# Performance work log

Measured on AMD Instinct MI355X. Metric: run time of the kernel, lower is better.

Reference implementation:

```python
import jax, jax.numpy as jnp
import numpy as np

N = 100000   # nodes
E = 1600000  # edges (avg degree 16)
D = 64       # input feature dim


def _lin(k, i, o):
    return (jax.random.normal(k, (i, o), jnp.float32) / np.float32(np.sqrt(i)))


def setup_inputs() -> dict:
    key = jax.random.key(0)
    ks = jax.random.split(key, 12)
    return {
        "x": jax.random.normal(ks[0], (N, D), jnp.float32),
        "edge_index": jax.random.randint(ks[1], (2, E), 0, N, dtype=jnp.int64),
        # layer 1: SAGEConv(64, 64, 'pool')
        "W1_pool": _lin(ks[2], 64, 64), "b1_pool": jnp.zeros((64,), jnp.float32),
        "W1_self": _lin(ks[3], 64, 64), "W1_neigh": _lin(ks[4], 64, 64),
        "b1": jnp.zeros((64,), jnp.float32),
        # layer 2: SAGEConv(64, 32, 'pool')
        "W2_pool": _lin(ks[5], 64, 64), "b2_pool": jnp.zeros((64,), jnp.float32),
        "W2_self": _lin(ks[6], 64, 32), "W2_neigh": _lin(ks[7], 64, 32),
        "b2": jnp.zeros((32,), jnp.float32),
        # layer 3: SAGEConv(32, 32, 'mean')
        "W3_self": _lin(ks[8], 32, 32), "W3_neigh": _lin(ks[9], 32, 32),
        "b3": jnp.zeros((32,), jnp.float32),
    }


def _sage_pool(x, src, dst, Wp, bp, Ws, Wn, b):
    # max-pool aggregator: transform all nodes once (cheaper than per-edge),
    # gather per-edge, segment-max into destination nodes.
    m = jax.nn.relu(x @ Wp + bp)[src]                      # [E, in]
    agg = jax.ops.segment_max(m, dst, num_segments=N)     # [N, in]
    agg = jnp.where(jnp.isfinite(agg), agg, jnp.float32(0.0))  # isolated nodes -> 0
    return x @ Ws + agg @ Wn + b


def _sage_mean(x, src, dst, Ws, Wn, b):
    s = jax.ops.segment_sum(x[src], dst, num_segments=N)   # [N, in]
    cnt = jax.ops.segment_sum(jnp.ones((src.shape[0],), jnp.float32), dst,
                              num_segments=N)
    agg = s / jnp.maximum(cnt, jnp.float32(1.0))[:, None]
    return x @ Ws + agg @ Wn + b


def reference(x, edge_index,
              W1_pool, b1_pool, W1_self, W1_neigh, b1,
              W2_pool, b2_pool, W2_self, W2_neigh, b2,
              W3_self, W3_neigh, b3):
    src, dst = edge_index[0], edge_index[1]
    h = jax.nn.relu(_sage_pool(x, src, dst, W1_pool, b1_pool, W1_self, W1_neigh, b1))
    h = _sage_pool(h, src, dst, W2_pool, b2_pool, W2_self, W2_neigh, b2)
    h = _sage_mean(h, src, dst, W3_self, W3_neigh, b3)
    return h
```

## Files before the change

kernel.cpp:

```cpp
#include <hip/hip_runtime.h>
#include <hip/hip_bf16.h>


typedef unsigned int uint;
typedef short short8 __attribute__((ext_vector_type(8)));
typedef float f32x4 __attribute__((ext_vector_type(4)));
typedef float f32x2 __attribute__((ext_vector_type(2)));
typedef unsigned short u16x8 __attribute__((ext_vector_type(8)));

__device__ __forceinline__ float bf2f(unsigned short h){
  return __uint_as_float(((uint)h) << 16);
}
__device__ __forceinline__ unsigned short f2bf(float f){
  uint u = __float_as_uint(f);
  u += 0x7fffu + ((u >> 16) & 1u);
  return (unsigned short)(u >> 16);
}
__device__ __forceinline__ float lo16(uint u){ return __uint_as_float(u << 16); }
__device__ __forceinline__ float hi16(uint u){ return __uint_as_float(u & 0xffff0000u); }

__device__ __forceinline__ uint4 pkmax4(uint4 a, uint4 b){
  u16x8 x = __builtin_bit_cast(u16x8, a);
  u16x8 y = __builtin_bit_cast(u16x8, b);
  return __builtin_bit_cast(uint4, __builtin_elementwise_max(x, y));
}
__device__ __forceinline__ uint4 shflx4(uint4 a, int off){
  uint4 r;
  r.x = (uint)__shfl_xor((int)a.x, off, 64);
  r.y = (uint)__shfl_xor((int)a.y, off, 64);
  r.z = (uint)__shfl_xor((int)a.z, off, 64);
  r.w = (uint)__shfl_xor((int)a.w, off, 64);
  return r;
}
__device__ __forceinline__ f32x2 b2lo(uint u){
  f32x2 r; r.x = lo16(u); r.y = hi16(u); return r;
}

struct WConv {
  const void* src[13];
  int n[13], isbias[13], Cs[13], K[13], off[13];
};

__global__ void conv_w(WConv wc, unsigned short* wtbase, float* bbase,
                       const unsigned short* x, const int* ei,
                       int* flags, int* ccur, int NB){
  __shared__ int sflags[2];
  int t = threadIdx.x;
  if (t < 64){
    int sane = 0;
    #pragma unroll
    for (int k = 0; k < 4; ++k){
      int e = (x[(t * 4 + k) * 2] >> 7) & 0xff;
      sane += (e >= 118 && e <= 134);
    }
    #pragma unroll
    for (int off = 32; off; off >>= 1) sane += __shfl_down(sane, off, 64);
    unsigned long long b = __ballot(ei[1 + 2 * t] != 0);
    if (t == 0){ sflags[0] = (sane >= 128); sflags[1] = (b == 0ull); }
  }
  __syncthreads();
  int isbf = sflags[0];
  if (blockIdx.x == 0){
    if (t == 0){ flags[0] = sflags[0]; flags[1] = sflags[1]; }
    for (int i = t; i < NB; i += 256) ccur[i] = 0;
  }
  int bt = blockIdx.x, n = wc.n[bt];
  if (wc.isbias[bt]){
    float* d = bbase + wc.off[bt];
    for (int i = t; i < n; i += 256)
      d[i] = isbf ? bf2f(((const unsigned short*)wc.src[bt])[i])
                  : ((const float*)wc.src[bt])[i];
  } else {
    unsigned short* d = wtbase + wc.off[bt];
    int Cs = wc.Cs[bt], K = wc.K[bt], Cm = (1 << Cs) - 1;
    for (int i = t; i < n; i += 256){
      int k = i >> Cs, c = i & Cm;
      unsigned short v = isbf ? ((const unsigned short*)wc.src[bt])[i]
                              : f2bf(((const float*)wc.src[bt])[i]);
      d[c * K + k] = v;
    }
  }
}

__device__ __forceinline__ void load_edge(const void* ei, int E, int is64, int e,
                                          int& s, int& d){
  if (is64){
    const long long* p = (const long long*)ei;
    s = (int)p[e]; d = (int)p[E + e];
  } else {
    const int* p = (const int*)ei;
    s = p[e]; d = p[E + e];
  }
}

__device__ __forceinline__ short8 ld_fragA_bf16(const unsigned short* A, int row,
                                                int K, int koff){
  return *(const short8*)(A + (size_t)row * K + koff);
}
__device__ __forceinline__ short8 ld_fragA_f32(const float* A, int row,
                                               int K, int koff){
  const float* q = A + (size_t)row * K + koff;
  float4 f0 = *(const float4*)q;
  float4 f1 = *(const float4*)(q + 4);
  short8 r;
  r[0] = (short)f2bf(f0.x); r[1] = (short)f2bf(f0.y);
  r[2] = (short)f2bf(f0.z); r[3] = (short)f2bf(f0.w);
  r[4] = (short)f2bf(f1.x); r[5] = (short)f2bf(f1.y);
  r[6] = (short)f2bf(f1.z); r[7] = (short)f2bf(f1.w);
  return r;
}
__device__ __forceinline__ unsigned short f2bf_relu(float f){
  return (unsigned short)(f2bf(fmaxf(f, 0.f)) & 0x7fff);
}

#define CSR_CE 2048

__device__ __forceinline__ void phase1_body(
    const void* __restrict__ ei, const int* __restrict__ flags,
    int* __restrict__ ccur, uint* __restrict__ pairs,
    int E, int N, int NB, int S, int CAP, int blk,
    uint* hist, uint* gbase)
{
  int t = threadIdx.x;
  uint dmask = (1u << S) - 1u;
  int is64 = flags[1];
  int e0 = blk * CSR_CE;
  for (int i = t; i < 1024; i += 256) hist[i] = 0;
  __syncthreads();
  uint pr[8]; short bb[8];
  #pragma unroll
  for (int k = 0; k < 8; ++k){
    int e = e0 + k * 256 + t;
    int s = 0, d = 0; bool ok = (e < E);
    if (ok){
      load_edge(ei, E, is64, e, s, d);
      ok = (unsigned)s < (unsigned)N && (unsigned)d < (unsigned)N;
    }
    bb[k] = ok ? (short)(d >> S) : (short)(-1);
    pr[k] = ((uint)s << S) | ((uint)d & dmask);
    if (ok) atomicAdd(&hist[d >> S], 1u);
  }
  __syncthreads();
  for (int b = t; b < NB; b += 256){
    uint c = hist[b];
    if (c) gbase[b] = (uint)atomicAdd(&ccur[b], (int)c);
    hist[b] = 0;
  }
  __syncthreads();
  #pragma unroll
  for (int k = 0; k < 8; ++k){
    int b = (int)bb[k];
    if (b >= 0){
      uint local = atomicAdd(&hist[b], 1u);
      uint pos = gbase[b] + local;
      if (pos >= (uint)CAP) pos = (uint)CAP - 1;
      pairs[(size_t)b * CAP + pos] = pr[k];
    }
  }
}

template<int AMODE>
__device__ __forceinline__ void mm1_body(
    const void* __restrict__ Av, const unsigned short* __restrict__ WaT,
    const float* __restrict__ bias, const int* __restrict__ flags,
    unsigned short* __restrict__ out, int N, int blk)
{
  int wid = threadIdx.x >> 6, lane = threadIdx.x & 63;
  int n0 = blk * 32;
  int m = lane & 15, quad = lane >> 4, koq = quad * 8;
  int colbase = wid * 16;
  int rowc0 = min(n0 + m, N - 1);
  int rowc1 = min(n0 + 16 + m, N - 1);
  bool af32 = (AMODE == 2) && (flags[0] == 0);
  f32x4 a0 = {0.f,0.f,0.f,0.f}, a1 = {0.f,0.f,0.f,0.f};
  #pragma unroll
  for (int k0 = 0; k0 < 64; k0 += 32){
    short8 af0 = af32 ? ld_fragA_f32((const float*)Av, rowc0, 64, k0 + koq)
                      : ld_fragA_bf16((const unsigned short*)Av, rowc0, 64, k0 + koq);
    short8 af1 = af32 ? ld_fragA_f32((const float*)Av, rowc1, 64, k0 + koq)
                      : ld_fragA_bf16((const unsigned short*)Av, rowc1, 64, k0 + koq);
    short8 wf = *(const short8*)(WaT + (size_t)(colbase + m) * 64 + k0 + koq);
    a0 = __builtin_amdgcn_mfma_f32_16x16x32_bf16(af0, wf, a0, 0, 0, 0);
    a1 = __builtin_amdgcn_mfma_f32_16x16x32_bf16(af1, wf, a1, 0, 0, 0);
  }
  float bv = bias[colbase + m];
  #pragma unroll
  for (int r = 0; r < 4; ++r){
    int rl = quad * 4 + r;
    if (n0 + rl < N)
      out[(size_t)(n0 + rl) * 64 + colbase + m] = f2bf_relu(a0[r] + bv);
    if (n0 + 16 + rl < N)
      out[(size_t)(n0 + 16 + rl) * 64 + colbase + m] = f2bf_relu(a1[r] + bv);
  }
}

template<int AMODE>
__global__ __launch_bounds__(256) void phase1_mm1(
    const void* __restrict__ ei, const int* __restrict__ flags,
    int* __restrict__ ccur, uint* __restrict__ pairs,
    int E, int N, int NB, int S, int CAP, int nP,
    const void* __restrict__ x, const unsigned short* __restrict__ W1pT,
    const float* __restrict__ b1p, unsigned short* __restrict__ mbuf)
{
  __shared__ uint hist[1024];
  __shared__ uint gbase[1024];
  if ((int)blockIdx.x < nP)
    phase1_body(ei, flags, ccur, pairs, E, N, NB, S, CAP, blockIdx.x, hist, gbase);
  else
    mm1_body<AMODE>(x, W1pT, b1p, flags, mbuf, N, blockIdx.x - nP);
}

__global__ void csr_scan0(const int* __restrict__ ccur, int* __restrict__ cbase,
                          int* __restrict__ rowptrN, int NB, int CAP)
{
  __shared__ int sm[256];
  int t = threadIdx.x;
  int g = (NB + 255) / 256;
  int vb = t * g, v[4], s = 0;
  for (int k = 0; k < g; ++k){
    int i = vb + k; int x = (i < NB) ? min(ccur[i], CAP) : 0; v[k] = x; s += x;
  }
  sm[t] = s; __syncthreads();
  for (int off = 1; off < 256; off <<= 1){
    int x = (t >= off) ? sm[t - off] : 0;
    __syncthreads(); sm[t] += x; __syncthreads();
  }
  int run = sm[t] - s;
  for (int k = 0; k < g; ++k){
    int i = vb + k;
    if (i < NB){ cbase[i] = run; run += v[k]; }
  }
  if (t == 255){ cbase[NB] = run; *rowptrN = run; }
}

#define P2_CAP 6144
__global__ __launch_bounds__(256) void csr_phase2(
    const int* __restrict__ cbase, const int* __restrict__ ccur,
    const uint* __restrict__ pairs,
    int* __restrict__ bucket, int* __restrict__ row_ptr, int N, int S, int CAP)
{
  __shared__ int lbuf[P2_CAP];
  __shared__ int cur[1024];
  __shared__ int sm[256];
  int b = blockIdx.x, t = threadIdx.x;
  uint dmask = (1u << S) - 1u;
  int n0 = b << S;
  int n1 = n0 + (1 << S); if (n1 > N) n1 = N;
  int nn = n1 - n0;
  int base = cbase[b];
  int cnt = min(ccur[b], CAP);
  const uint* bp = pairs + (size_t)b * CAP;

  for (int i = t; i < nn; i += 256) cur[i] = 0;
  __syncthreads();
  for (int j = t; j < cnt; j += 256)
    atomicAdd(&cur[(int)(bp[j] & dmask)], 1);
  __syncthreads();
  int g = (nn + 255) / 256, vb = t * g, v[4], s = 0;
  for (int k = 0; k < g; ++k){
    int i = vb + k; int x = (i < nn) ? cur[i] : 0; v[k] = x; s += x;
  }
  sm[t] = s; __syncthreads();
  for (int off = 1; off < 256; off <<= 1){
    int x = (t >= off) ? sm[t - off] : 0;
    __syncthreads(); sm[t] += x; __syncthreads();
  }
  int run = sm[t] - s;
  for (int k = 0; k < g; ++k){
    int i = vb + k;
    if (i < nn){ row_ptr[n0 + i] = base + run; cur[i] = run; run += v[k]; }
  }
  __syncthreads();
  if (cnt <= 0) return;
  if (cnt <= P2_CAP){
    for (int j = t; j < cnt; j += 256){
      uint pr = bp[j];
      int pos = atomicAdd(&cur[(int)(pr & dmask)], 1);
      lbuf[pos] = (int)(pr >> S);
    }
    __syncthreads();
    for (int i = t; i < cnt; i += 256) bucket[base + i] = lbuf[i];
  } else {
    for (int j = t; j < cnt; j += 256){
      uint pr = bp[j];
      int pos = atomicAdd(&cur[(int)(pr & dmask)], 1);
      bucket[base + pos] = (int)(pr >> S);
    }
  }
}

__global__ __launch_bounds__(256) void gather_max64(
    const int* __restrict__ row_ptr, const int* __restrict__ bucket,
    const unsigned short* __restrict__ m, unsigned short* __restrict__ agg, int N)
{
  int wave = (int)((blockIdx.x * 256u + threadIdx.x) >> 6);
  int lane = threadIdx.x & 63;
  int nodeA = wave * 2, nodeB = nodeA + 1;
  if (nodeA >= N) return;
  bool hasB = nodeB < N;
  int rsA = row_ptr[nodeA], reA = row_ptr[nodeA + 1];
  int cntA = reA - rsA;
  int rsB = reA, cntB = hasB ? (row_ptr[nodeB + 1] - reA) : 0;
  int fg8 = (lane & 7) * 8, rowsel = lane >> 3;
  uint4 accA = {0u,0u,0u,0u}, accB = {0u,0u,0u,0u};
  int cmax = max(cntA, cntB);
  for (int c0 = 0; c0 < cmax; c0 += 64){
    int chA = min(cntA - c0, 64);
    int chB = min(cntB - c0, 64);
    int bvA = (lane < chA) ? bucket[rsA + c0 + lane] : 0;
    int bvB = (lane < chB) ? bucket[rsB + c0 + lane] : 0;
    int it = (max(chA, chB) + 7) >> 3;
    for (int k = 0; k < it; ++k){
      int j = k * 8 + rowsel;
      int sA = __shfl(bvA, j, 64);
      int sB = __shfl(bvB, j, 64);
      uint4 vA = *(const uint4*)(m + (size_t)sA * 64 + fg8);
      uint4 vB = *(const uint4*)(m + (size_t)sB * 64 + fg8);
      if (j < chA) accA = pkmax4(accA, vA);
      if (j < chB) accB = pkmax4(accB, vB);
    }
  }
  #pragma unroll
  for (int off = 8; off <= 32; off <<= 1){
    accA = pkmax4(accA, shflx4(accA, off));
    accB = pkmax4(accB, shflx4(accB, off));
  }
  if (lane < 8){
    *(uint4*)(agg + (size_t)nodeA * 64 + fg8) = accA;
  } else if (lane < 16 && hasB){
    *(uint4*)(agg + (size_t)nodeB * 64 + (lane & 7) * 8) = accB;
  }
}

template<int AMODE>
__global__ __launch_bounds__(256) void mfma_mm_fused(
    const void* __restrict__ Av, const unsigned short* __restrict__ Bv,
    const unsigned short* __restrict__ WaT, const unsigned short* __restrict__ WbT,
    const float* __restrict__ bias1,
    const unsigned short* __restrict__ WcT, const float* __restrict__ bias2,
    const int* __restrict__ flags,
    unsigned short* __restrict__ out1, unsigned short* __restrict__ out2, int N)
{
  constexpr int K = 64, C = 64, LDH = 72;
  __shared__ unsigned short hl[32 * LDH];
  int wid = threadIdx.x >> 6, lane = threadIdx.x & 63;
  int n0 = blockIdx.x * 32;
  int m = lane & 15, quad = lane >> 4, koq = quad * 8;
  int colbase = wid * 16;
  int rowc0 = min(n0 + m, N - 1);
  int rowc1 = min(n0 + 16 + m, N - 1);
  bool af32 = (AMODE == 2) && (flags[0] == 0);

  f32x4 a0 = {0.f,0.f,0.f,0.f}, a1 = {0.f,0.f,0.f,0.f};
  #pragma unroll
  for (int k0 = 0; k0 < K; k0 += 32){
    short8 af0 = af32 ? ld_fragA_f32((const float*)Av, rowc0, K, k0 + koq)
                      : ld_fragA_bf16((const unsigned short*)Av, rowc0, K, k0 + koq);
    short8 af1 = af32 ? ld_fragA_f32((const float*)Av, rowc1, K, k0 + koq)
                      : ld_fragA_bf16((const unsigned short*)Av, rowc1, K, k0 + koq);
    short8 wf = *(const short8*)(WaT + (size_t)(colbase + m) * K + k0 + koq);
    a0 = __builtin_amdgcn_mfma_f32_16x16x32_bf16(af0, wf, a0, 0, 0, 0);
    a1 = __builtin_amdgcn_mfma_f32_16x16x32_bf16(af1, wf, a1, 0, 0, 0);
    short8 bf0 = ld_fragA_bf16(Bv, rowc0, K, k0 + koq);
    short8 bf1 = ld_fragA_bf16(Bv, rowc1, K, k0 + koq);
    short8 wg = *(const short8*)(WbT + (size_t)(colbase + m) * K + k0 + koq);
    a0 = __builtin_amdgcn_mfma_f32_16x16x32_bf16(bf0, wg, a0, 0, 0, 0);
    a1 = __builtin_amdgcn_mfma_f32_16x16x32_bf16(bf1, wg, a1, 0, 0, 0);
  }
  float bv = bias1[colbase + m];
  #pragma unroll
  for (int r = 0; r < 4; ++r){
    int rl = quad * 4 + r;
    unsigned short h0 = f2bf_relu(a0[r] + bv);
    unsigned short h1v = f2bf_relu(a1[r] + bv);
    hl[rl * LDH + colbase + m] = h0;
    hl[(16 + rl) * LDH + colbase + m] = h1v;
    if (n0 + rl < N) out1[(size_t)(n0 + rl) * C + colbase + m] = h0;
    if (n0 + 16 + rl < N) out1[(size_t)(n0 + 16 + rl) * C + colbase + m] = h1v;
  }
  __syncthreads();
  f32x4 c0 = {0.f,0.f,0.f,0.f}, c1 = {0.f,0.f,0.f,0.f};
  #pragma unroll
  for (int k0 = 0; k0 < K; k0 += 32){
    short8 q0 = *(const short8*)(hl + m * LDH + k0 + koq);
    short8 q1 = *(const short8*)(hl + (16 + m) * LDH + k0 + koq);
    short8 wf = *(const short8*)(WcT + (size_t)(colbase + m) * K + k0 + koq);
    c0 = __builtin_amdgcn_mfma_f32_16x16x32_bf16(q0, wf, c0, 0, 0, 0);
    c1 = __builtin_amdgcn_mfma_f32_16x16x32_bf16(q1, wf, c1, 0, 0, 0);
  }
  float b2v = bias2[colbase + m];
  #pragma unroll
  for (int r = 0; r < 4; ++r){
    int rl = quad * 4 + r;
    if (n0 + rl < N)
      out2[(size_t)(n0 + rl) * C + colbase + m] = f2bf_relu(c0[r] + b2v);
    if (n0 + 16 + rl < N)
      out2[(size_t)(n0 + 16 + rl) * C + colbase + m] = f2bf_relu(c1[r] + b2v);
  }
}

__global__ __launch_bounds__(256) void mfma_mm2(
    const unsigned short* __restrict__ h1, const unsigned short* __restrict__ aggb,
    const unsigned short* __restrict__ WsT, const unsigned short* __restrict__ WnT,
    const float* __restrict__ bias, unsigned short* __restrict__ h2, int N)
{
  int wid = threadIdx.x >> 6, lane = threadIdx.x & 63;
  int n0 = blockIdx.x * 64 + (wid >> 1) * 32;
  int colbase = (wid & 1) * 16;
  int m = lane & 15, quad = lane >> 4, koq = quad * 8;
  int rowc0 = min(n0 + m, N - 1), rowc1 = min(n0 + 16 + m, N - 1);
  f32x4 a0 = {0.f,0.f,0.f,0.f}, a1 = {0.f,0.f,0.f,0.f};
  #pragma unroll
  for (int k0 = 0; k0 < 64; k0 += 32){
    short8 af0 = *(const short8*)(h1 + (size_t)rowc0 * 64 + k0 + koq);
    short8 af1 = *(const short8*)(h1 + (size_t)rowc1 * 64 + k0 + koq);
    short8 wf = *(const short8*)(WsT + (size_t)(colbase + m) * 64 + k0 + koq);
    a0 = __builtin_amdgcn_mfma_f32_16x16x32_bf16(af0, wf, a0, 0, 0, 0);
    a1 = __builtin_amdgcn_mfma_f32_16x16x32_bf16(af1, wf, a1, 0, 0, 0);
    short8 bf0 = *(const short8*)(aggb + (size_t)rowc0 * 64 + k0 + koq);
    short8 bf1 = *(const short8*)(aggb + (size_t)rowc1 * 64 + k0 + koq);
    short8 wg = *(const short8*)(WnT + (size_t)(colbase + m) * 64 + k0 + koq);
    a0 = __builtin_amdgcn_mfma_f32_16x16x32_bf16(bf0, wg, a0, 0, 0, 0);
    a1 = __builtin_amdgcn_mfma_f32_16x16x32_bf16(bf1, wg, a1, 0, 0, 0);
  }
  float bv = bias[colbase + m];
  #pragma unroll
  for (int r = 0; r < 4; ++r){
    int rl = quad * 4 + r;
    if (n0 + rl < N)
      h2[(size_t)(n0 + rl) * 32 + colbase + m] = f2bf(a0[r] + bv);
    if (n0 + 16 + rl < N)
      h2[(size_t)(n0 + 16 + rl) * 32 + colbase + m] = f2bf(a1[r] + bv);
  }
}

__global__ __launch_bounds__(256) void gsum3(
    const int* __restrict__ row_ptr, const int* __restrict__ bucket,
    const unsigned short* __restrict__ h2,
    const unsigned short* __restrict__ W3sT, const unsigned short* __restrict__ W3nT,
    const float* __restrict__ b3, float* __restrict__ out, int N)
{
  constexpr int LDA = 40;
  __shared__ unsigned short la[16 * LDA];
  int t = threadIdx.x;
  int w = t >> 6, lane = t & 63;
  int n0 = blockIdx.x * 16;
  int g = lane >> 4, q = lane & 15;
  int nd = n0 + w * 4 + g;
  int ndc = nd < N ? nd : N - 1;
  int rs = row_ptr[ndc];
  int cnt = (nd < N) ? (row_ptr[ndc + 1] - rs) : 0;
  int fg8 = (q & 3) * 8, rowsel = q >> 2;
  f32x2 a0 = {0.f,0.f}, a1 = {0.f,0.f}, a2 = {0.f,0.f}, a3 = {0.f,0.f};
  for (int c0 = 0; c0 < cnt; c0 += 16){
    int chunk = min(cnt - c0, 16);
    int bval = (q < chunk) ? bucket[rs + c0 + q] : 0;
    int it = (chunk + 3) >> 2;
    for (int k = 0; k < it; ++k){
      int j = k * 4 + rowsel;
      int s = __shfl(bval, (g << 4) + j, 64);
      uint4 v = *(const uint4*)(h2 + (size_t)s * 32 + fg8);
      if (j < chunk){
        a0 += b2lo(v.x); a1 += b2lo(v.y); a2 += b2lo(v.z); a3 += b2lo(v.w);
      }
    }
  }
  #pragma unroll
  for (int off = 4; off <= 8; off <<= 1){
    a0.x += __shfl_xor(a0.x, off, 64); a0.y += __shfl_xor(a0.y, off, 64);
    a1.x += __shfl_xor(a1.x, off, 64); a1.y += __shfl_xor(a1.y, off, 64);
    a2.x += __shfl_xor(a2.x, off, 64); a2.y += __shfl_xor(a2.y, off, 64);
    a3.x += __shfl_xor(a3.x, off, 64); a3.y += __shfl_xor(a3.y, off, 64);
  }
  if (rowsel == 0){
    float sc = 1.f / fmaxf((float)cnt, 1.f);
    int r = w * 4 + g;
    uint4 pk;
    pk.x = (uint)f2bf(a0.x * sc) | ((uint)f2bf(a0.y * sc) << 16);
    pk.y = (uint)f2bf(a1.x * sc) | ((uint)f2bf(a1.y * sc) << 16);
    pk.z = (uint)f2bf(a2.x * sc) | ((uint)f2bf(a2.y * sc) << 16);
    pk.w = (uint)f2bf(a3.x * sc) | ((uint)f2bf(a3.y * sc) << 16);
    *(uint4*)(la + r * LDA + q * 8) = pk;
  }
  __syncthreads();
  if (w < 2){
    int m = lane & 15, quad = lane >> 4, koq = quad * 8;
    int colbase = w * 16;
    int row = n0 + m;
    int rowc = row < N ? row : N - 1;
    f32x4 acc = {0.f, 0.f, 0.f, 0.f};
    short8 aself = *(const short8*)(h2 + (size_t)rowc * 32 + koq);
    short8 wfs = *(const short8*)(W3sT + (size_t)(colbase + m) * 32 + koq);
    acc = __builtin_amdgcn_mfma_f32_16x16x32_bf16(aself, wfs, acc, 0, 0, 0);
    short8 aagg = *(const short8*)(la + m * LDA + koq);
    short8 wfn = *(const short8*)(W3nT + (size_t)(colbase + m) * 32 + koq);
    acc = __builtin_amdgcn_mfma_f32_16x16x32_bf16(aagg, wfn, acc, 0, 0, 0);
    float bv = b3[colbase + m];
    #pragma unroll
    for (int r = 0; r < 4; ++r){
      int orow = n0 + quad * 4 + r;
      if (orow < N) out[(size_t)orow * 32 + colbase + m] = acc[r] + bv;
    }
  }
}

static inline char* align256(char* p){
  return (char*)(((uintptr_t)p + 255) & ~(uintptr_t)255);
}

extern "C" void kernel_launch(void* const* d_in, const int* in_sizes, int n_in,
                              void* d_out, int out_size, void* d_ws, size_t ws_size,
                              hipStream_t stream)
{
  const void* x = d_in[0];
  const void* ei = d_in[1];
  int N = in_sizes[0] / 64;
  int E = in_sizes[1] / 2;

  char* ws = (char*)d_ws;
  unsigned short* wtbase = (unsigned short*)ws;
  float* bbase = (float*)(ws + 65536);
  int* flags = (int*)(ws + 131072 - 256);

  int S = 7, NB = (N + 127) >> 7;
  while (NB > 1024){ S++; NB = (N + (1 << S) - 1) >> S; }
  int CAP = ((2 * E / NB) + 255) & ~255;
  if (CAP < 1024) CAP = 1024;

  char* p = ws + 131072;
  int* row_ptr = (int*)p; p = align256(p + (size_t)(N + 1) * 4);
  int* cbase   = (int*)p; p = align256(p + 4352);
  int* ccur    = (int*)p; p = align256(p + 4352);
  int* bucket  = (int*)p; p = align256(p + (size_t)E * 4);
  uint* pairs  = (uint*)p; p = align256(p + (size_t)NB * CAP * 4);
  char* P = p;  p = align256(p + (size_t)N * 64 * 2);
  char* Q = p;  p = align256(p + (size_t)N * 64 * 2);
  char* R = p;  p = align256(p + (size_t)N * 64 * 2);
  unsigned short* mbuf = (unsigned short*)P;
  unsigned short* h2   = (unsigned short*)P;
  unsigned short* aggb = (unsigned short*)Q;
  unsigned short* h1   = (unsigned short*)R;

  WConv wc;
  {
    const int widx[13] = {2, 3, 4, 5, 6, 7, 8, 9, 10, 11, 12, 13, 14};
    const int isb[13]  = {0, 1, 0, 0, 1, 0, 1, 0, 0, 1, 0, 0, 1};
    const int Cs[13]   = {6, 0, 6, 6, 0, 6, 0, 5, 5, 0, 5, 5, 0};
    const int Kk[13]   = {64, 0, 64, 64, 0, 64, 0, 64, 64, 0, 32, 32, 0};
    const int off[13]  = {0, 0, 4096, 8192, 64, 12288, 128, 16384, 18432, 192,
                          20480, 21504, 224};
    for (int i = 0; i < 13; ++i){
      wc.src[i] = d_in[widx[i]]; wc.n[i] = in_sizes[widx[i]];
      wc.isbias[i] = isb[i]; wc.Cs[i] = Cs[i]; wc.K[i] = Kk[i]; wc.off[i] = off[i];
    }
  }
  hipLaunchKernelGGL(conv_w, dim3(13), dim3(256), 0, stream, wc, wtbase, bbase,
                     (const unsigned short*)x, (const int*)ei, flags, ccur, NB);
  unsigned short* W1pT = wtbase + 0;     unsigned short* W1sT = wtbase + 4096;
  unsigned short* W1nT = wtbase + 8192;  unsigned short* W2pT = wtbase + 12288;
  unsigned short* W2sT = wtbase + 16384; unsigned short* W2nT = wtbase + 18432;
  unsigned short* W3sT = wtbase + 20480; unsigned short* W3nT = wtbase + 21504;
  float* b1p = bbase + 0;  float* b1 = bbase + 64; float* b2p = bbase + 128;
  float* b2 = bbase + 192; float* b3 = bbase + 224;

  int nP = (E + CSR_CE - 1) / CSR_CE;
  int RT32 = (N + 31) / 32;
  int RT16 = (N + 15) / 16;
  int gg = (N + 7) / 8;

  phase1_mm1<2><<<nP + RT32, 256, 0, stream>>>(
      ei, flags, ccur, pairs, E, N, NB, S, CAP, nP, x, W1pT, b1p, mbuf);
  csr_scan0<<<1, 256, 0, stream>>>(ccur, cbase, row_ptr + N, NB, CAP);
  csr_phase2<<<NB, 256, 0, stream>>>(cbase, ccur, pairs, bucket, row_ptr, N, S, CAP);

  gather_max64<<<gg,256,0,stream>>>(row_ptr, bucket, mbuf, aggb, N);
  mfma_mm_fused<2><<<RT32,256,0,stream>>>(
      x, aggb, W1sT, W1nT, b1, W2pT, b2p, flags, h1, mbuf, N);

  gather_max64<<<gg,256,0,stream>>>(row_ptr, bucket, mbuf, aggb, N);
  mfma_mm2<<<(N + 63) / 64,256,0,stream>>>(h1, aggb, W2sT, W2nT, b2, h2, N);

  gsum3<<<RT16,256,0,stream>>>(row_ptr, bucket, h2, W3sT, W3nT, b3,
                               (float*)d_out, N);
}
```

Measured before the change: 292.3 us.

## Fuse max-gather into matmul kernels and enlarge CSR edge chunks

The two standalone gather_max64 kernels are folded into the following MFMA matmul kernels. Each block now gathers its own rows' neighbour max into shared memory and reads the aggregated operand from LDS, so the agg buffer no longer makes a global round trip and two launches are dropped. The layer-2 message buffer moves to its own allocation because m1 is read while m2 is written. CSR phase 1 now handles 8192 edges per block and re-reads edges in its second pass instead of holding them in registers, which means fewer blocks and fewer global atomics but twice the edge reads and less parallelism.

```diff
diff --git a/kernel.cpp b/kernel.cpp
--- a/kernel.cpp
+++ b/kernel.cpp
@@ -113,7 +113,7 @@
   return (unsigned short)(f2bf(fmaxf(f, 0.f)) & 0x7fff);
 }
 
-#define CSR_CE 2048
+#define CSR_CE 8192
 
 __device__ __forceinline__ void phase1_body(
     const void* __restrict__ ei, const int* __restrict__ flags,
@@ -127,18 +127,13 @@
   int e0 = blk * CSR_CE;
   for (int i = t; i < 1024; i += 256) hist[i] = 0;
   __syncthreads();
-  uint pr[8]; short bb[8];
-  #pragma unroll
-  for (int k = 0; k < 8; ++k){
-    int e = e0 + k * 256 + t;
-    int s = 0, d = 0; bool ok = (e < E);
-    if (ok){
-      load_edge(ei, E, is64, e, s, d);
-      ok = (unsigned)s < (unsigned)N && (unsigned)d < (unsigned)N;
-    }
-    bb[k] = ok ? (short)(d >> S) : (short)(-1);
-    pr[k] = ((uint)s << S) | ((uint)d & dmask);
-    if (ok) atomicAdd(&hist[d >> S], 1u);
+  #pragma unroll 4
+  for (int it = 0; it < CSR_CE / 256; ++it){
+    int e = e0 + it * 256 + t;
+    if (e >= E) break;
+    int s, d; load_edge(ei, E, is64, e, s, d);
+    if ((unsigned)s >= (unsigned)N || (unsigned)d >= (unsigned)N) continue;
+    atomicAdd(&hist[d >> S], 1u);
   }
   __syncthreads();
   for (int b = t; b < NB; b += 256){
@@ -147,15 +142,17 @@
     hist[b] = 0;
   }
   __syncthreads();
-  #pragma unroll
-  for (int k = 0; k < 8; ++k){
-    int b = (int)bb[k];
-    if (b >= 0){
-      uint local = atomicAdd(&hist[b], 1u);
-      uint pos = gbase[b] + local;
-      if (pos >= (uint)CAP) pos = (uint)CAP - 1;
-      pairs[(size_t)b * CAP + pos] = pr[k];
-    }
+  #pragma unroll 4
+  for (int it = 0; it < CSR_CE / 256; ++it){
+    int e = e0 + it * 256 + t;
+    if (e >= E) break;
+    int s, d; load_edge(ei, E, is64, e, s, d);
+    if ((unsigned)s >= (unsigned)N || (unsigned)d >= (unsigned)N) continue;
+    int b = d >> S;
+    uint local = atomicAdd(&hist[b], 1u);
+    uint pos = gbase[b] + local;
+    if (pos >= (uint)CAP) pos = (uint)CAP - 1;
+    pairs[(size_t)b * CAP + pos] = ((uint)s << S) | ((uint)d & dmask);
   }
 }
 
@@ -289,18 +286,17 @@
   }
 }
 
-__global__ __launch_bounds__(256) void gather_max64(
+__device__ __forceinline__ void gmax_pair(
     const int* __restrict__ row_ptr, const int* __restrict__ bucket,
-    const unsigned short* __restrict__ m, unsigned short* __restrict__ agg, int N)
-{
-  int wave = (int)((blockIdx.x * 256u + threadIdx.x) >> 6);
-  int lane = threadIdx.x & 63;
-  int nodeA = wave * 2, nodeB = nodeA + 1;
-  if (nodeA >= N) return;
-  bool hasB = nodeB < N;
-  int rsA = row_ptr[nodeA], reA = row_ptr[nodeA + 1];
-  int cntA = reA - rsA;
-  int rsB = reA, cntB = hasB ? (row_ptr[nodeB + 1] - reA) : 0;
+    const unsigned short* __restrict__ m,
+    unsigned short* la_row, int LDH, int nodeA, int N, int lane)
+{
+  int nodeB = nodeA + 1;
+  int nAc = min(nodeA, N - 1);
+  int rsA = row_ptr[nAc], reA = row_ptr[nAc + 1];
+  int cntA = (nodeA < N) ? (reA - rsA) : 0;
+  int rsB = reA;
+  int cntB = (nodeB < N) ? (row_ptr[nodeB + 1] - reA) : 0;
   int fg8 = (lane & 7) * 8, rowsel = lane >> 3;
   uint4 accA = {0u,0u,0u,0u}, accB = {0u,0u,0u,0u};
   int cmax = max(cntA, cntB);
@@ -326,15 +322,16 @@
     accB = pkmax4(accB, shflx4(accB, off));
   }
   if (lane < 8){
-    *(uint4*)(agg + (size_t)nodeA * 64 + fg8) = accA;
-  } else if (lane < 16 && hasB){
-    *(uint4*)(agg + (size_t)nodeB * 64 + (lane & 7) * 8) = accB;
+    *(uint4*)(la_row + fg8) = accA;
+  } else if (lane < 16){
+    *(uint4*)(la_row + LDH + (lane & 7) * 8) = accB;
   }
 }
 
 template<int AMODE>
-__global__ __launch_bounds__(256) void mfma_mm_fused(
-    const void* __restrict__ Av, const unsigned short* __restrict__ Bv,
+__global__ __launch_bounds__(256) void gmax_mm_fused(
+    const void* __restrict__ Av, const unsigned short* __restrict__ msrc,
+    const int* __restrict__ row_ptr, const int* __restrict__ bucket,
     const unsigned short* __restrict__ WaT, const unsigned short* __restrict__ WbT,
     const float* __restrict__ bias1,
     const unsigned short* __restrict__ WcT, const float* __restrict__ bias2,
@@ -342,9 +339,16 @@
     unsigned short* __restrict__ out1, unsigned short* __restrict__ out2, int N)
 {
   constexpr int K = 64, C = 64, LDH = 72;
+  __shared__ unsigned short la[32 * LDH];
   __shared__ unsigned short hl[32 * LDH];
   int wid = threadIdx.x >> 6, lane = threadIdx.x & 63;
   int n0 = blockIdx.x * 32;
+  #pragma unroll
+  for (int p = 0; p < 4; ++p){
+    int lr = wid * 8 + p * 2;
+    gmax_pair(row_ptr, bucket, msrc, la + (size_t)lr * LDH, LDH, n0 + lr, N, lane);
+  }
+  __syncthreads();
   int m = lane & 15, quad = lane >> 4, koq = quad * 8;
   int colbase = wid * 16;
   int rowc0 = min(n0 + m, N - 1);
@@ -361,8 +365,8 @@
     short8 wf = *(const short8*)(WaT + (size_t)(colbase + m) * K + k0 + koq);
     a0 = __builtin_amdgcn_mfma_f32_16x16x32_bf16(af0, wf, a0, 0, 0, 0);
     a1 = __builtin_amdgcn_mfma_f32_16x16x32_bf16(af1, wf, a1, 0, 0, 0);
-    short8 bf0 = ld_fragA_bf16(Bv, rowc0, K, k0 + koq);
-    short8 bf1 = ld_fragA_bf16(Bv, rowc1, K, k0 + koq);
+    short8 bf0 = *(const short8*)(la + m * LDH + k0 + koq);
+    short8 bf1 = *(const short8*)(la + (16 + m) * LDH + k0 + koq);
     short8 wg = *(const short8*)(WbT + (size_t)(colbase + m) * K + k0 + koq);
     a0 = __builtin_amdgcn_mfma_f32_16x16x32_bf16(bf0, wg, a0, 0, 0, 0);
     a1 = __builtin_amdgcn_mfma_f32_16x16x32_bf16(bf1, wg, a1, 0, 0, 0);
@@ -399,16 +403,26 @@
   }
 }
 
-__global__ __launch_bounds__(256) void mfma_mm2(
-    const unsigned short* __restrict__ h1, const unsigned short* __restrict__ aggb,
+__global__ __launch_bounds__(256) void gmax_mm2(
+    const unsigned short* __restrict__ h1, const unsigned short* __restrict__ msrc,
+    const int* __restrict__ row_ptr, const int* __restrict__ bucket,
     const unsigned short* __restrict__ WsT, const unsigned short* __restrict__ WnT,
     const float* __restrict__ bias, unsigned short* __restrict__ h2, int N)
 {
+  constexpr int LDH = 72;
+  __shared__ unsigned short la[64 * LDH];
   int wid = threadIdx.x >> 6, lane = threadIdx.x & 63;
-  int n0 = blockIdx.x * 64 + (wid >> 1) * 32;
+  int n0 = blockIdx.x * 64;
+  #pragma unroll
+  for (int p = 0; p < 8; ++p){
+    int lr = wid * 16 + p * 2;
+    gmax_pair(row_ptr, bucket, msrc, la + (size_t)lr * LDH, LDH, n0 + lr, N, lane);
+  }
+  __syncthreads();
+  int m = lane & 15, quad = lane >> 4, koq = quad * 8;
   int colbase = (wid & 1) * 16;
-  int m = lane & 15, quad = lane >> 4, koq = quad * 8;
-  int rowc0 = min(n0 + m, N - 1), rowc1 = min(n0 + 16 + m, N - 1);
+  int rb = (wid >> 1) * 32;
+  int rowc0 = min(n0 + rb + m, N - 1), rowc1 = min(n0 + rb + 16 + m, N - 1);
   f32x4 a0 = {0.f,0.f,0.f,0.f}, a1 = {0.f,0.f,0.f,0.f};
   #pragma unroll
   for (int k0 = 0; k0 < 64; k0 += 32){
@@ -417,8 +431,8 @@
     short8 wf = *(const short8*)(WsT + (size_t)(colbase + m) * 64 + k0 + koq);
     a0 = __builtin_amdgcn_mfma_f32_16x16x32_bf16(af0, wf, a0, 0, 0, 0);
     a1 = __builtin_amdgcn_mfma_f32_16x16x32_bf16(af1, wf, a1, 0, 0, 0);
-    short8 bf0 = *(const short8*)(aggb + (size_t)rowc0 * 64 + k0 + koq);
-    short8 bf1 = *(const short8*)(aggb + (size_t)rowc1 * 64 + k0 + koq);
+    short8 bf0 = *(const short8*)(la + (rb + m) * LDH + k0 + koq);
+    short8 bf1 = *(const short8*)(la + (rb + 16 + m) * LDH + k0 + koq);
     short8 wg = *(const short8*)(WnT + (size_t)(colbase + m) * 64 + k0 + koq);
     a0 = __builtin_amdgcn_mfma_f32_16x16x32_bf16(bf0, wg, a0, 0, 0, 0);
     a1 = __builtin_amdgcn_mfma_f32_16x16x32_bf16(bf1, wg, a1, 0, 0, 0);
@@ -427,10 +441,10 @@
   #pragma unroll
   for (int r = 0; r < 4; ++r){
     int rl = quad * 4 + r;
-    if (n0 + rl < N)
-      h2[(size_t)(n0 + rl) * 32 + colbase + m] = f2bf(a0[r] + bv);
-    if (n0 + 16 + rl < N)
-      h2[(size_t)(n0 + 16 + rl) * 32 + colbase + m] = f2bf(a1[r] + bv);
+    if (n0 + rb + rl < N)
+      h2[(size_t)(n0 + rb + rl) * 32 + colbase + m] = f2bf(a0[r] + bv);
+    if (n0 + rb + 16 + rl < N)
+      h2[(size_t)(n0 + rb + 16 + rl) * 32 + colbase + m] = f2bf(a1[r] + bv);
   }
 }
 
@@ -536,10 +550,10 @@
   char* P = p;  p = align256(p + (size_t)N * 64 * 2);
   char* Q = p;  p = align256(p + (size_t)N * 64 * 2);
   char* R = p;  p = align256(p + (size_t)N * 64 * 2);
-  unsigned short* mbuf = (unsigned short*)P;
-  unsigned short* h2   = (unsigned short*)P;
-  unsigned short* aggb = (unsigned short*)Q;
-  unsigned short* h1   = (unsigned short*)R;
+  unsigned short* m1 = (unsigned short*)P;
+  unsigned short* h2 = (unsigned short*)P;
+  unsigned short* m2 = (unsigned short*)Q;
+  unsigned short* h1 = (unsigned short*)R;
 
   WConv wc;
   {
@@ -566,19 +580,17 @@
   int nP = (E + CSR_CE - 1) / CSR_CE;
   int RT32 = (N + 31) / 32;
   int RT16 = (N + 15) / 16;
-  int gg = (N + 7) / 8;
 
   phase1_mm1<2><<<nP + RT32, 256, 0, stream>>>(
-      ei, flags, ccur, pairs, E, N, NB, S, CAP, nP, x, W1pT, b1p, mbuf);
+      ei, flags, ccur, pairs, E, N, NB, S, CAP, nP, x, W1pT, b1p, m1);
   csr_scan0<<<1, 256, 0, stream>>>(ccur, cbase, row_ptr + N, NB, CAP);
   csr_phase2<<<NB, 256, 0, stream>>>(cbase, ccur, pairs, bucket, row_ptr, N, S, CAP);
 
-  gather_max64<<<gg,256,0,stream>>>(row_ptr, bucket, mbuf, aggb, N);
-  mfma_mm_fused<2><<<RT32,256,0,stream>>>(
-      x, aggb, W1sT, W1nT, b1, W2pT, b2p, flags, h1, mbuf, N);
-
-  gather_max64<<<gg,256,0,stream>>>(row_ptr, bucket, mbuf, aggb, N);
-  mfma_mm2<<<(N + 63) / 64,256,0,stream>>>(h1, aggb, W2sT, W2nT, b2, h2, N);
+  gmax_mm_fused<2><<<RT32,256,0,stream>>>(
+      x, m1, row_ptr, bucket, W1sT, W1nT, b1, W2pT, b2p, flags, h1, m2, N);
+
+  gmax_mm2<<<(N + 63) / 64,256,0,stream>>>(
+      h1, m2, row_ptr, bucket, W2sT, W2nT, b2, h2, N);
 
   gsum3<<<RT16,256,0,stream>>>(row_ptr, bucket, h2, W3sT, W3nT, b3,
                                (float*)d_out, N);
```

After: 274.0 us. 6.3% less time.
